# Performance work log

Measured on AMD Instinct MI355X. Metric: run time of the kernel, lower is better.

The kernel has to match this reference:

```python
import jax, jax.numpy as jnp
import numpy as np
from jax import lax

B, T, V, E, H = 32, 512, 32000, 300, 256
TRANSITION = 0.1
TEMP = 0.01
BUDGET_PCT = 30.0
NEG = -1e9


def setup_inputs() -> dict:
    key = jax.random.key(0)
    ks = jax.random.split(key, 10)
    sc = lambda k, shape, s=0.05: (jax.random.normal(k, shape, jnp.float32) * s)
    x = jax.random.randint(ks[0], (B, T), 0, V)
    mask = jnp.ones((B, T), bool)
    embed = sc(ks[1], (V, E), 0.1)
    w_ih_f = sc(ks[2], (E, 4 * H))
    w_hh_f = sc(ks[3], (H, 4 * H))
    b_f = jnp.zeros((4 * H,), jnp.float32)
    w_ih_b = sc(ks[4], (E, 4 * H))
    w_hh_b = sc(ks[5], (H, 4 * H))
    b_b = jnp.zeros((4 * H,), jnp.float32)
    w_out = sc(ks[6], (2 * H, 1), 0.1)
    b_out = jnp.zeros((1,), jnp.float32)
    return {"x": x, "current_epoch": 0, "mask": mask, "embed": embed,
            "w_ih_f": w_ih_f, "w_hh_f": w_hh_f, "b_f": b_f,
            "w_ih_b": w_ih_b, "w_hh_b": w_hh_b, "b_b": b_b,
            "w_out": w_out, "b_out": b_out}


def _lstm_dir(emb, mask, Wi, Wh, b):
    # masked LSTM equivalent to pack_padded_sequence; gate order i,f,g,o (torch)
    bs, tl, _ = emb.shape
    h0 = jnp.zeros((bs, Wh.shape[0]), emb.dtype)
    xg = emb @ Wi + b  # [B,T,4H]

    def step(carry, inp):
        h, c = carry
        xg_t, m_t = inp
        g = xg_t + h @ Wh
        i, f, gg, o = jnp.split(g, 4, axis=-1)
        i = jax.nn.sigmoid(i); f = jax.nn.sigmoid(f)
        gg = jnp.tanh(gg); o = jax.nn.sigmoid(o)
        c_new = f * c + i * gg
        h_new = o * jnp.tanh(c_new)
        m = m_t[:, None]
        h_new = jnp.where(m, h_new, h)
        c_new = jnp.where(m, c_new, c)
        return (h_new, c_new), jnp.where(m, h_new, 0.0)

    _, hs = lax.scan(step, (h0, h0), (xg.transpose(1, 0, 2), mask.T))
    return hs.transpose(1, 0, 2)


def _forward(x, mask, embed, w_ih_f, w_hh_f, b_f, w_ih_b, w_hh_b, b_b, w_out, b_out):
    emb = embed[x]  # [B,T,E] (dropout disabled / eval)
    h_f = _lstm_dir(emb, mask, w_ih_f, w_hh_f, b_f)
    h_b = jnp.flip(_lstm_dir(jnp.flip(emb, 1), jnp.flip(mask, 1), w_ih_b, w_hh_b, b_b), 1)
    h = jnp.concatenate([h_f, h_b], axis=-1)  # [B,T,2H]
    scores = (h @ w_out + b_out)[..., 0]  # [B,T]

    lengths = mask.sum(1)
    pos = jnp.arange(T)
    # unary for state 0 (selected); padded positions forced off
    u0 = jnp.where(pos[None, :] < lengths[:, None], scores / TEMP, NEG)
    # transition[t,0,0] = transition/temp for t <= length, else 0;  t in 0..T
    tvals = jnp.where(jnp.arange(T + 1)[None, :] <= lengths[:, None], TRANSITION / TEMP, 0.0)
    budget = jnp.round(BUDGET_PCT / 100.0 * lengths)
    Cmax = int(round(BUDGET_PCT / 100.0 * T)) + 1  # static count dim

    def logZ(u0_):
        alpha = jnp.full((u0_.shape[0], Cmax, 2), NEG, u0_.dtype)
        alpha = alpha.at[:, 1, 0].set(u0_[:, 0] + tvals[:, 0])  # start in state0 (count 1)
        alpha = alpha.at[:, 0, 1].set(0.0)                       # start in state1 (count 0)

        def step(a, inp):
            u0_t, t_t = inp
            a_shift = jnp.concatenate([jnp.full((a.shape[0], 1, 2), NEG, a.dtype), a[:, :-1, :]], axis=1)
            m0 = jnp.logaddexp(a_shift[..., 0] + t_t[:, None], a_shift[..., 1])
            m1 = jnp.logaddexp(a[..., 0], a[..., 1])
            return jnp.stack([u0_t[:, None] + m0, m1], axis=-1), None

        alpha, _ = lax.scan(step, alpha, (u0_[:, 1:].T, tvals[:, 1:T].T))
        final = jnp.stack([alpha[..., 0] + tvals[:, T][:, None], alpha[..., 1]], axis=-1)
        allowed = (jnp.arange(Cmax)[None, :] <= budget[:, None])[..., None]
        lz = jax.nn.logsumexp(jnp.where(allowed, final, NEG).reshape(final.shape[0], -1), axis=-1)
        return lz.sum()

    # marginal p(z_i=1) = d logZ / d u0_i  (budget-constrained chain marginals)
    z = jax.grad(logZ)(u0)
    return jnp.where(mask, z, 0.0)


def reference(x, current_epoch, mask, embed, w_ih_f, w_hh_f, b_f, w_ih_b, w_hh_b, b_b, w_out, b_out):
    return _forward(x, mask, embed, w_ih_f, w_hh_f, b_f, w_ih_b, w_hh_b, b_b, w_out, b_out)
```

## Files before the change

### kernel.cpp

```cpp
#include <hip/hip_runtime.h>
#include <math.h>

#define BB 32
#define TT_LEN 512
#define EE 300
#define KPAD 320
#define HH 256
#define G4 1024
#define CMAX 155
#define TRANS_T 10.0f
#define NEGF -1.0e9f
#define INV_TEMP 100.0f
#define AST_STRIDE 160

#define NCH_L2 8
#define NREG 24

typedef _Float16 half2v __attribute__((ext_vector_type(2)));
typedef _Float16 half8 __attribute__((ext_vector_type(8)));
typedef float f32x4 __attribute__((ext_vector_type(4)));

__device__ __forceinline__ float la(float x, float y) {
  float m = fmaxf(x, y);
  float d = fminf(x, y) - m;
  return m + __logf(1.0f + __expf(d));
}

__device__ __forceinline__ float sigm(float x) {
  return 1.0f / (1.0f + __expf(-x));
}

__device__ __forceinline__ float dot2acc(unsigned int wd, unsigned int hd, float acc) {
#if __has_builtin(__builtin_amdgcn_fdot2)
  return __builtin_amdgcn_fdot2(__builtin_bit_cast(half2v, wd),
                                __builtin_bit_cast(half2v, hd), acc, false);
#else
  half2v a = __builtin_bit_cast(half2v, wd);
  half2v b = __builtin_bit_cast(half2v, hd);
  return acc + (float)a.x * (float)b.x + (float)a.y * (float)b.y;
#endif
}

__device__ __forceinline__ unsigned int packh(float a, float b) {
  half2v hp;
  hp.x = (_Float16)a;
  hp.y = (_Float16)b;
  return __builtin_bit_cast(unsigned int, hp);
}

__global__ void prep_weights(const float* wi_f, const float* wi_b,
                             const float* wh_f, const float* wh_b,
                             const float* b_f, const float* b_b,
                             _Float16* wi_t, float* b_p,
                             unsigned int* wlds_h, unsigned int* wstr_h) {
  int idx = blockIdx.x * blockDim.x + threadIdx.x;
  int stride = gridDim.x * blockDim.x;
  for (int i = idx; i < 2 * G4 * KPAD; i += stride) {
    int dir = i / (G4 * KPAD);
    int r = i % (G4 * KPAD);
    int j = r / KPAD;
    int k = r % KPAD;
    int g = j & 3, u = j >> 2;
    const float* src = dir ? wi_b : wi_f;
    wi_t[i] = (k < EE) ? (_Float16)src[(size_t)k * G4 + g * HH + u] : (_Float16)0.0f;
  }
  for (int i = idx; i < 2 * NCH_L2 * 4096; i += stride) {
    int dir = i / (NCH_L2 * 4096);
    int r = i % (NCH_L2 * 4096);
    int c = r / 4096;
    int r2 = r % 4096;
    int j = r2 >> 2, d = r2 & 3;
    int g = j & 3, u = j >> 2;
    int k0 = 8 * c + 2 * d;
    const float* src = dir ? wh_b : wh_f;
    wlds_h[i] = packh(src[k0 * G4 + g * HH + u], src[(k0 + 1) * G4 + g * HH + u]);
  }
  for (int i = idx; i < 2 * NREG * 4096; i += stride) {
    int dir = i / (NREG * 4096);
    int r = i % (NREG * 4096);
    int gch = r / 4096;
    int r2 = r % 4096;
    int j = r2 >> 2, d = r2 & 3;
    int g = j & 3, u = j >> 2;
    int k0 = 64 + 8 * gch + 2 * d;
    const float* src = dir ? wh_b : wh_f;
    wstr_h[i] = packh(src[k0 * G4 + g * HH + u], src[(k0 + 1) * G4 + g * HH + u]);
  }
  for (int i = idx; i < 2 * G4; i += stride) {
    int dir = i / G4;
    int j = i % G4;
    int g = j & 3, u = j >> 2;
    const float* src = dir ? b_b : b_f;
    b_p[i] = src[g * HH + u];
  }
}

__global__ void gather_emb(const int* x, const float* embed, _Float16* emb_h) {
  int row = blockIdx.x;
  int v = x[row];
  const float* src = embed + (size_t)v * EE;
  _Float16* dst = emb_h + (size_t)row * KPAD;
  for (int k = threadIdx.x; k < KPAD; k += blockDim.x)
    dst[k] = (k < EE) ? (_Float16)src[k] : (_Float16)0.0f;
}

__global__ __launch_bounds__(256) void xg_mfma(
    const _Float16* __restrict__ emb_h, const _Float16* __restrict__ wi_t,
    const float* __restrict__ b_p, float* __restrict__ xg) {
  int dir = blockIdx.z;
  int n0 = blockIdx.x * 64;
  int m0 = blockIdx.y * 64;
  int wave = threadIdx.x >> 6;
  int lane = threadIdx.x & 63;
  int l15 = lane & 15, quad = lane >> 4;

  const _Float16* arow = emb_h + (size_t)(m0 + wave * 16 + l15) * KPAD + quad * 8;
  const _Float16* bbase =
      wi_t + ((size_t)dir * G4 + n0 + l15) * KPAD + quad * 8;

  f32x4 acc[4];
#pragma unroll
  for (int nt = 0; nt < 4; ++nt) acc[nt] = (f32x4){0.f, 0.f, 0.f, 0.f};

#pragma unroll
  for (int kk = 0; kk < KPAD / 32; ++kk) {
    half8 a = *(const half8*)(arow + kk * 32);
#pragma unroll
    for (int nt = 0; nt < 4; ++nt) {
      half8 b = *(const half8*)(bbase + (size_t)nt * 16 * KPAD + kk * 32);
      acc[nt] = __builtin_amdgcn_mfma_f32_16x16x32_f16(a, b, acc[nt], 0, 0, 0);
    }
  }
#pragma unroll
  for (int nt = 0; nt < 4; ++nt) {
    int n = n0 + nt * 16 + l15;
    float bias = b_p[dir * G4 + n];
#pragma unroll
    for (int r = 0; r < 4; ++r) {
      int m = m0 + wave * 16 + quad * 4 + r;
      xg[((size_t)dir * (BB * TT_LEN) + m) * G4 + n] = acc[nt][r] + bias;
    }
  }
}

__global__ __launch_bounds__(512, 2) void lstm_reg(
    const float* __restrict__ xg, const unsigned int* __restrict__ wlds_h,
    const uint4* __restrict__ wstr, const float* __restrict__ w_out,
    float* __restrict__ scores_part) {
  int bid = blockIdx.x;
  int dir = bid >> 5, b = bid & 31;
  int t = threadIdx.x;
  int lane = t & 63, wid = t >> 6;

  __shared__ uint4 wlds[NCH_L2 * 1024];
  __shared__ uint4 hpk4[32];
  __shared__ float gates[1024];
  __shared__ float wpart[2][4];

  const uint4* wsrcl = (const uint4*)wlds_h + (size_t)dir * (NCH_L2 * 1024);
  for (int i = t; i < NCH_L2 * 1024; i += 512) wlds[i] = wsrcl[i];
  const uint4* wsb = wstr + (size_t)dir * (NREG * 1024);
  uint4 wr0[NREG], wr1[NREG];
#pragma unroll
  for (int g = 0; g < NREG; ++g) {
    wr0[g] = wsb[g * 1024 + t];
    wr1[g] = wsb[g * 1024 + t + 512];
  }
  if (t < 32) hpk4[t] = uint4{0, 0, 0, 0};
  __syncthreads();

  const float* xgbase =
      xg + (size_t)(dir * (BB * TT_LEN) + b * TT_LEN) * G4 + t;
  float wo = (t < HH) ? w_out[dir * HH + t] : 0.0f;
  float cstate = 0.0f;

  int t0 = dir ? (TT_LEN - 1) : 0;
  float xgn0 = xgbase[(size_t)t0 * G4];
  float xgn1 = xgbase[(size_t)t0 * G4 + 512];

#pragma unroll 1
  for (int s = 0; s < TT_LEN; ++s) {
    int tt = dir ? (TT_LEN - 1 - s) : s;
    float acc0 = xgn0, acc1 = xgn1;
    if (s + 1 < TT_LEN) {
      int t2 = dir ? (TT_LEN - 2 - s) : (s + 1);
      xgn0 = xgbase[(size_t)t2 * G4];
      xgn1 = xgbase[(size_t)t2 * G4 + 512];
    }
#pragma unroll
    for (int c = 0; c < NCH_L2; ++c) {
      uint4 h = hpk4[c];
      uint4 w0 = wlds[c * 1024 + t];
      uint4 w1 = wlds[c * 1024 + 512 + t];
      acc0 = dot2acc(w0.x, h.x, acc0);
      acc0 = dot2acc(w0.y, h.y, acc0);
      acc0 = dot2acc(w0.z, h.z, acc0);
      acc0 = dot2acc(w0.w, h.w, acc0);
      acc1 = dot2acc(w1.x, h.x, acc1);
      acc1 = dot2acc(w1.y, h.y, acc1);
      acc1 = dot2acc(w1.z, h.z, acc1);
      acc1 = dot2acc(w1.w, h.w, acc1);
    }
#pragma unroll
    for (int g = 0; g < NREG; ++g) {
      uint4 h = hpk4[NCH_L2 + g];
      acc0 = dot2acc(wr0[g].x, h.x, acc0);
      acc0 = dot2acc(wr0[g].y, h.y, acc0);
      acc0 = dot2acc(wr0[g].z, h.z, acc0);
      acc0 = dot2acc(wr0[g].w, h.w, acc0);
      acc1 = dot2acc(wr1[g].x, h.x, acc1);
      acc1 = dot2acc(wr1[g].y, h.y, acc1);
      acc1 = dot2acc(wr1[g].z, h.z, acc1);
      acc1 = dot2acc(wr1[g].w, h.w, acc1);
    }
    gates[t] = acc0;
    gates[512 + t] = acc1;
    __syncthreads();

    if (t < HH) {
      float4 g4 = ((const float4*)gates)[t];
      float ig = sigm(g4.x);
      float fg = sigm(g4.y);
      float gg = tanhf(g4.z);
      float og = sigm(g4.w);
      cstate = fg * cstate + ig * gg;
      float h = og * tanhf(cstate);
      float prod = h * wo;
#pragma unroll
      for (int off = 32; off > 0; off >>= 1) prod += __shfl_down(prod, off, 64);
      if (lane == 0) wpart[s & 1][wid] = prod;
      float hn = __shfl_down(h, 1, 64);
      if (!(t & 1)) ((unsigned int*)hpk4)[t >> 1] = packh(h, hn);
    }
    __syncthreads();
    if (t == 0) {
      scores_part[(size_t)(dir * BB + b) * TT_LEN + tt] =
          wpart[s & 1][0] + wpart[s & 1][1] + wpart[s & 1][2] + wpart[s & 1][3];
    }
  }
}

__global__ __launch_bounds__(64) void dp2(const float* __restrict__ scores_part,
                                          const float* __restrict__ b_out,
                                          float* __restrict__ ast_g,
                                          float* __restrict__ out) {
  int b = blockIdx.x;
  int l = threadIdx.x;
  const float* spf = scores_part + (size_t)b * TT_LEN;
  const float* spb = scores_part + (size_t)(BB + b) * TT_LEN;
  float bo = b_out[0];
  float* ast = ast_g + (size_t)b * TT_LEN * AST_STRIDE;

  float ur[8];
#pragma unroll
  for (int i = 0; i < 8; ++i)
    ur[i] = (spf[i * 64 + l] + spb[i * 64 + l] + bo) * INV_TEMP;

  int lm1 = (l + 63) & 63;
  int lp1 = (l + 1) & 63;

  float a0[3], a1[3];
  float u00 = __shfl(ur[0], 0, 64);
  a0[0] = (l == 1) ? (u00 + TRANS_T) : NEGF;
  a0[1] = NEGF;
  a0[2] = NEGF;
  a1[0] = (l == 0) ? 0.0f : NEGF;
  a1[1] = NEGF;
  a1[2] = NEGF;
  ast[l] = a0[0];
  ast[64 + l] = a0[1];
  if (l < 27) ast[128 + l] = a0[2];

#pragma unroll
  for (int ch = 0; ch < 8; ++ch) {
    float uc = ur[ch];
#pragma unroll 1
    for (int tt = (ch == 0 ? 1 : 0); tt < 64; ++tt) {
      int t = ch * 64 + tt;
      float u0t = __shfl(uc, tt, 64);
      float w0a = __shfl(a0[0], lm1, 64);
      float w1a = __shfl(a0[1], lm1, 64);
      float w2a = __shfl(a0[2], lm1, 64);
      float w0b = __shfl(a1[0], lm1, 64);
      float w1b = __shfl(a1[1], lm1, 64);
      float w2b = __shfl(a1[2], lm1, 64);
      float p0a = (l == 0) ? NEGF : w0a;
      float p1a = (l == 0) ? w0a : w1a;
      float p2a = (l == 0) ? w1a : w2a;
      float p0b = (l == 0) ? NEGF : w0b;
      float p1b = (l == 0) ? w0b : w1b;
      float p2b = (l == 0) ? w1b : w2b;
      float n00 = u0t + la(p0a + TRANS_T, p0b);
      float n01 = u0t + la(p1a + TRANS_T, p1b);
      float n02 = u0t + la(p2a + TRANS_T, p2b);
      float n10 = la(a0[0], a1[0]);
      float n11 = la(a0[1], a1[1]);
      float n12 = la(a0[2], a1[2]);
      a0[0] = n00;
      a0[1] = n01;
      a0[2] = (l < 27) ? n02 : NEGF;
      a1[0] = n10;
      a1[1] = n11;
      a1[2] = (l < 27) ? n12 : NEGF;
      float* astr = ast + (size_t)t * AST_STRIDE;
      astr[l] = a0[0];
      astr[64 + l] = a0[1];
      if (l < 27) astr[128 + l] = a0[2];
    }
  }

  float f00 = a0[0] + TRANS_T, f01 = a0[1] + TRANS_T, f02 = a0[2] + TRANS_T;
  float m = fmaxf(fmaxf(fmaxf(f00, f01), fmaxf(f02, a1[0])), fmaxf(a1[1], a1[2]));
#pragma unroll
  for (int off = 32; off > 0; off >>= 1) m = fmaxf(m, __shfl_xor(m, off, 64));
  float es = __expf(f00 - m) + __expf(f01 - m) + __expf(f02 - m) +
             __expf(a1[0] - m) + __expf(a1[1] - m) + __expf(a1[2] - m);
#pragma unroll
  for (int off = 32; off > 0; off >>= 1) es += __shfl_xor(es, off, 64);
  float lz = m + __logf(es);

  float b0[3], b1[3];
  b0[0] = TRANS_T;
  b0[1] = TRANS_T;
  b0[2] = (l < 27) ? TRANS_T : NEGF;
  b1[0] = 0.0f;
  b1[1] = 0.0f;
  b1[2] = (l < 27) ? 0.0f : NEGF;
  {
    float ts = __expf(a0[0] + TRANS_T - lz) + __expf(a0[1] + TRANS_T - lz) +
               ((l < 27) ? __expf(a0[2] + TRANS_T - lz) : 0.0f);
#pragma unroll
    for (int off = 32; off > 0; off >>= 1) ts += __shfl_xor(ts, off, 64);
    if (l == 0) out[b * TT_LEN + (TT_LEN - 1)] = ts;
  }

  float nr0 = ast[(size_t)510 * AST_STRIDE + l];
  float nr1 = ast[(size_t)510 * AST_STRIDE + 64 + l];
  float nr2 = (l < 27) ? ast[(size_t)510 * AST_STRIDE + 128 + l] : NEGF;

#pragma unroll
  for (int ch = 7; ch >= 0; --ch) {
    float uc = ur[ch];
#pragma unroll 1
    for (int tt = 63; tt >= (ch == 0 ? 1 : 0); --tt) {
      int t = ch * 64 + tt;
      float u0t = __shfl(uc, tt, 64);
      float c0 = nr0, c1 = nr1, c2 = nr2;
      if (t >= 2) {
        const float* astr = ast + (size_t)(t - 2) * AST_STRIDE;
        nr0 = astr[l];
        nr1 = astr[64 + l];
        nr2 = (l < 27) ? astr[128 + l] : NEGF;
      }
      float w0 = __shfl(b0[0], lp1, 64);
      float w1 = __shfl(b0[1], lp1, 64);
      float w2 = __shfl(b0[2], lp1, 64);
      float x2 = (l == 63) ? NEGF : w2;
      float x1 = (l == 63) ? w2 : w1;
      float x0 = (l == 63) ? w1 : w0;
      float nb00 = la(u0t + TRANS_T + x0, b1[0]);
      float nb01 = la(u0t + TRANS_T + x1, b1[1]);
      float nb02 = la(u0t + TRANS_T + x2, b1[2]);
      float nb10 = la(u0t + x0, b1[0]);
      float nb11 = la(u0t + x1, b1[1]);
      float nb12 = la(u0t + x2, b1[2]);
      float tm = __expf(c0 + nb00 - lz) + __expf(c1 + nb01 - lz) +
                 ((l < 27) ? __expf(c2 + nb02 - lz) : 0.0f);
#pragma unroll
      for (int off = 32; off > 0; off >>= 1) tm += __shfl_xor(tm, off, 64);
      if (l == 0) out[b * TT_LEN + (t - 1)] = tm;
      b0[0] = nb00;
      b0[1] = nb01;
      b0[2] = (l < 27) ? nb02 : NEGF;
      b1[0] = nb10;
      b1[1] = nb11;
      b1[2] = (l < 27) ? nb12 : NEGF;
    }
  }
}

extern "C" void kernel_launch(void* const* d_in, const int* in_sizes, int n_in,
                              void* d_out, int out_size, void* d_ws, size_t ws_size,
                              hipStream_t stream) {
  const int* x = (const int*)d_in[0];
  const float* embed = (const float*)d_in[3];
  const float* wi_f = (const float*)d_in[4];
  const float* wh_f = (const float*)d_in[5];
  const float* bf = (const float*)d_in[6];
  const float* wi_b = (const float*)d_in[7];
  const float* wh_b = (const float*)d_in[8];
  const float* bbias = (const float*)d_in[9];
  const float* w_out = (const float*)d_in[10];
  const float* b_out = (const float*)d_in[11];

  float* ws = (float*)d_ws;
  float* b_p = ws;
  unsigned int* wlds_h = (unsigned int*)(b_p + 2 * G4);
  unsigned int* wstr_h = wlds_h + 2 * NCH_L2 * 4096;
  _Float16* wi_t = (_Float16*)(wstr_h + 2 * NREG * 4096);
  _Float16* emb_h = wi_t + (size_t)2 * G4 * KPAD;
  float* xg = (float*)(emb_h + (size_t)BB * TT_LEN * KPAD);
  float* scores_part = xg + (size_t)2 * BB * TT_LEN * G4;
  float* u0_unused = scores_part + 2 * BB * TT_LEN;
  float* ast_g = u0_unused + BB * TT_LEN;
  float* outp = (float*)d_out;

  prep_weights<<<256, 256, 0, stream>>>(wi_f, wi_b, wh_f, wh_b, bf, bbias,
                                        wi_t, b_p, wlds_h, wstr_h);
  gather_emb<<<BB * TT_LEN, 256, 0, stream>>>(x, embed, emb_h);
  dim3 g1(G4 / 64, (BB * TT_LEN) / 64, 2);
  xg_mfma<<<g1, 256, 0, stream>>>(emb_h, wi_t, b_p, xg);
  lstm_reg<<<64, 512, 0, stream>>>(xg, wlds_h, (const uint4*)wstr_h, w_out,
                                   scores_part);
  dp2<<<BB, 64, 0, stream>>>(scores_part, b_out, ast_g, outp);
}
```

Before: 1.900 ms.

## Pre-swizzle MFMA fragments, split LSTM accumulators, chunk recurrence into four launches

Input weights and gathered embeddings are now written directly in MFMA fragment order, so the xg GEMM loads each operand as one coalesced uint4 per lane instead of strided half8 rows. The LSTM recurrence uses two accumulator chains per gate row to shorten the dependent dot2 chain. It is also split into four launches of 128 steps each, with h and c saved to and restored from global memory between chunks. The AST stride changes from 160 to 159, likely to avoid LDS or cache bank conflicts in the DP. Chunking adds launch overhead and reloads all register and LDS weights four times, which may cost more than it gains.

```diff
diff --git a/kernel.cpp b/kernel.cpp
--- a/kernel.cpp
+++ b/kernel.cpp
@@ -11,7 +11,7 @@
 #define TRANS_T 10.0f
 #define NEGF -1.0e9f
 #define INV_TEMP 100.0f
-#define AST_STRIDE 160
+#define AST_STRIDE 159
 
 #define NCH_L2 8
 #define NREG 24
@@ -51,18 +51,24 @@
 __global__ void prep_weights(const float* wi_f, const float* wi_b,
                              const float* wh_f, const float* wh_b,
                              const float* b_f, const float* b_b,
-                             _Float16* wi_t, float* b_p,
+                             unsigned int* wi_frag, float* b_p,
                              unsigned int* wlds_h, unsigned int* wstr_h) {
   int idx = blockIdx.x * blockDim.x + threadIdx.x;
   int stride = gridDim.x * blockDim.x;
-  for (int i = idx; i < 2 * G4 * KPAD; i += stride) {
-    int dir = i / (G4 * KPAD);
-    int r = i % (G4 * KPAD);
-    int j = r / KPAD;
-    int k = r % KPAD;
-    int g = j & 3, u = j >> 2;
+  for (int i = idx; i < 2 * 64 * 10 * 64 * 4; i += stride) {
+    int u4 = i >> 2, d = i & 3;
+    int lane = u4 & 63;
+    int kk = (u4 >> 6) % 10;
+    int nb = (u4 / 640) & 63;
+    int dir = u4 / (640 * 64);
+    int l15 = lane & 15, quad = lane >> 4;
+    int n = nb * 16 + l15;
+    int g = n & 3, u = n >> 2;
+    int k0 = kk * 32 + quad * 8 + 2 * d;
     const float* src = dir ? wi_b : wi_f;
-    wi_t[i] = (k < EE) ? (_Float16)src[(size_t)k * G4 + g * HH + u] : (_Float16)0.0f;
+    float v0 = (k0 < EE) ? src[(size_t)k0 * G4 + g * HH + u] : 0.0f;
+    float v1 = (k0 + 1 < EE) ? src[(size_t)(k0 + 1) * G4 + g * HH + u] : 0.0f;
+    wi_frag[i] = packh(v0, v1);
   }
   for (int i = idx; i < 2 * NCH_L2 * 4096; i += stride) {
     int dir = i / (NCH_L2 * 4096);
@@ -95,58 +101,73 @@
   }
 }
 
-__global__ void gather_emb(const int* x, const float* embed, _Float16* emb_h) {
-  int row = blockIdx.x;
-  int v = x[row];
-  const float* src = embed + (size_t)v * EE;
-  _Float16* dst = emb_h + (size_t)row * KPAD;
-  for (int k = threadIdx.x; k < KPAD; k += blockDim.x)
-    dst[k] = (k < EE) ? (_Float16)src[k] : (_Float16)0.0f;
+__global__ void gather_emb(const int* x, const float* embed, uint4* emb_frag) {
+  int mblk = blockIdx.x;
+  int t = threadIdx.x;
+  __shared__ int xs[16];
+  if (t < 16) xs[t] = x[mblk * 16 + t];
+  __syncthreads();
+  for (int slot = t; slot < 640; slot += 256) {
+    int kk = slot >> 6;
+    int lane = slot & 63;
+    int l15 = lane & 15, quad = lane >> 4;
+    int row = xs[l15];
+    int kbase = kk * 32 + quad * 8;
+    const float* src = embed + (size_t)row * EE;
+    float v[8];
+#pragma unroll
+    for (int e = 0; e < 8; ++e) v[e] = (kbase + e < EE) ? src[kbase + e] : 0.0f;
+    uint4 o;
+    o.x = packh(v[0], v[1]);
+    o.y = packh(v[2], v[3]);
+    o.z = packh(v[4], v[5]);
+    o.w = packh(v[6], v[7]);
+    emb_frag[(size_t)(mblk * 10 + kk) * 64 + lane] = o;
+  }
 }
 
 __global__ __launch_bounds__(256) void xg_mfma(
-    const _Float16* __restrict__ emb_h, const _Float16* __restrict__ wi_t,
+    const uint4* __restrict__ emb_frag, const uint4* __restrict__ wi_frag,
     const float* __restrict__ b_p, float* __restrict__ xg) {
   int dir = blockIdx.z;
-  int n0 = blockIdx.x * 64;
-  int m0 = blockIdx.y * 64;
-  int wave = threadIdx.x >> 6;
+  int w = threadIdx.x >> 6;
   int lane = threadIdx.x & 63;
   int l15 = lane & 15, quad = lane >> 4;
-
-  const _Float16* arow = emb_h + (size_t)(m0 + wave * 16 + l15) * KPAD + quad * 8;
-  const _Float16* bbase =
-      wi_t + ((size_t)dir * G4 + n0 + l15) * KPAD + quad * 8;
-
+  int mblk = blockIdx.y * 4 + w;
+
+  const uint4* abase = emb_frag + (size_t)mblk * 10 * 64 + lane;
   f32x4 acc[4];
 #pragma unroll
   for (int nt = 0; nt < 4; ++nt) acc[nt] = (f32x4){0.f, 0.f, 0.f, 0.f};
 
 #pragma unroll
-  for (int kk = 0; kk < KPAD / 32; ++kk) {
-    half8 a = *(const half8*)(arow + kk * 32);
+  for (int kk = 0; kk < 10; ++kk) {
+    half8 a = __builtin_bit_cast(half8, abase[kk * 64]);
 #pragma unroll
     for (int nt = 0; nt < 4; ++nt) {
-      half8 b = *(const half8*)(bbase + (size_t)nt * 16 * KPAD + kk * 32);
+      int nb = blockIdx.x * 4 + nt;
+      half8 b = __builtin_bit_cast(
+          half8, wi_frag[((size_t)(dir * 64 + nb) * 10 + kk) * 64 + lane]);
       acc[nt] = __builtin_amdgcn_mfma_f32_16x16x32_f16(a, b, acc[nt], 0, 0, 0);
     }
   }
 #pragma unroll
   for (int nt = 0; nt < 4; ++nt) {
-    int n = n0 + nt * 16 + l15;
+    int n = (blockIdx.x * 4 + nt) * 16 + l15;
     float bias = b_p[dir * G4 + n];
 #pragma unroll
     for (int r = 0; r < 4; ++r) {
-      int m = m0 + wave * 16 + quad * 4 + r;
+      int m = mblk * 16 + quad * 4 + r;
       xg[((size_t)dir * (BB * TT_LEN) + m) * G4 + n] = acc[nt][r] + bias;
     }
   }
 }
 
-__global__ __launch_bounds__(512, 2) void lstm_reg(
+__global__ __launch_bounds__(512, 2) void lstm_ck(
     const float* __restrict__ xg, const unsigned int* __restrict__ wlds_h,
     const uint4* __restrict__ wstr, const float* __restrict__ w_out,
-    float* __restrict__ scores_part) {
+    float* __restrict__ scores_part, float* __restrict__ hst,
+    float* __restrict__ cst, int s0i, int s1i) {
   int bid = blockIdx.x;
   int dir = bid >> 5, b = bid & 31;
   int t = threadIdx.x;
@@ -166,22 +187,25 @@
     wr0[g] = wsb[g * 1024 + t];
     wr1[g] = wsb[g * 1024 + t + 512];
   }
-  if (t < 32) hpk4[t] = uint4{0, 0, 0, 0};
+  if (t < 32)
+    hpk4[t] = (s0i == 0) ? uint4{0, 0, 0, 0} : ((const uint4*)hst)[bid * 32 + t];
+  float cstate = 0.0f;
+  if (s0i > 0 && t < HH) cstate = cst[bid * HH + t];
   __syncthreads();
 
   const float* xgbase =
       xg + (size_t)(dir * (BB * TT_LEN) + b * TT_LEN) * G4 + t;
   float wo = (t < HH) ? w_out[dir * HH + t] : 0.0f;
-  float cstate = 0.0f;
-
-  int t0 = dir ? (TT_LEN - 1) : 0;
+
+  int t0 = dir ? (TT_LEN - 1 - s0i) : s0i;
   float xgn0 = xgbase[(size_t)t0 * G4];
   float xgn1 = xgbase[(size_t)t0 * G4 + 512];
 
 #pragma unroll 1
-  for (int s = 0; s < TT_LEN; ++s) {
+  for (int s = s0i; s < s1i; ++s) {
     int tt = dir ? (TT_LEN - 1 - s) : s;
-    float acc0 = xgn0, acc1 = xgn1;
+    float acc0a = xgn0, acc1a = xgn1;
+    float acc0b = 0.0f, acc1b = 0.0f;
     if (s + 1 < TT_LEN) {
       int t2 = dir ? (TT_LEN - 2 - s) : (s + 1);
       xgn0 = xgbase[(size_t)t2 * G4];
@@ -192,29 +216,40 @@
       uint4 h = hpk4[c];
       uint4 w0 = wlds[c * 1024 + t];
       uint4 w1 = wlds[c * 1024 + 512 + t];
-      acc0 = dot2acc(w0.x, h.x, acc0);
-      acc0 = dot2acc(w0.y, h.y, acc0);
-      acc0 = dot2acc(w0.z, h.z, acc0);
-      acc0 = dot2acc(w0.w, h.w, acc0);
-      acc1 = dot2acc(w1.x, h.x, acc1);
-      acc1 = dot2acc(w1.y, h.y, acc1);
-      acc1 = dot2acc(w1.z, h.z, acc1);
-      acc1 = dot2acc(w1.w, h.w, acc1);
+      acc0a = dot2acc(w0.x, h.x, acc0a);
+      acc0a = dot2acc(w0.y, h.y, acc0a);
+      acc0a = dot2acc(w0.z, h.z, acc0a);
+      acc0a = dot2acc(w0.w, h.w, acc0a);
+      acc1a = dot2acc(w1.x, h.x, acc1a);
+      acc1a = dot2acc(w1.y, h.y, acc1a);
+      acc1a = dot2acc(w1.z, h.z, acc1a);
+      acc1a = dot2acc(w1.w, h.w, acc1a);
     }
 #pragma unroll
     for (int g = 0; g < NREG; ++g) {
       uint4 h = hpk4[NCH_L2 + g];
-      acc0 = dot2acc(wr0[g].x, h.x, acc0);
-      acc0 = dot2acc(wr0[g].y, h.y, acc0);
-      acc0 = dot2acc(wr0[g].z, h.z, acc0);
-      acc0 = dot2acc(wr0[g].w, h.w, acc0);
-      acc1 = dot2acc(wr1[g].x, h.x, acc1);
-      acc1 = dot2acc(wr1[g].y, h.y, acc1);
-      acc1 = dot2acc(wr1[g].z, h.z, acc1);
-      acc1 = dot2acc(wr1[g].w, h.w, acc1);
-    }
-    gates[t] = acc0;
-    gates[512 + t] = acc1;
+      if (g < 12) {
+        acc0a = dot2acc(wr0[g].x, h.x, acc0a);
+        acc0a = dot2acc(wr0[g].y, h.y, acc0a);
+        acc0a = dot2acc(wr0[g].z, h.z, acc0a);
+        acc0a = dot2acc(wr0[g].w, h.w, acc0a);
+        acc1a = dot2acc(wr1[g].x, h.x, acc1a);
+        acc1a = dot2acc(wr1[g].y, h.y, acc1a);
+        acc1a = dot2acc(wr1[g].z, h.z, acc1a);
+        acc1a = dot2acc(wr1[g].w, h.w, acc1a);
+      } else {
+        acc0b = dot2acc(wr0[g].x, h.x, acc0b);
+        acc0b = dot2acc(wr0[g].y, h.y, acc0b);
+        acc0b = dot2acc(wr0[g].z, h.z, acc0b);
+        acc0b = dot2acc(wr0[g].w, h.w, acc0b);
+        acc1b = dot2acc(wr1[g].x, h.x, acc1b);
+        acc1b = dot2acc(wr1[g].y, h.y, acc1b);
+        acc1b = dot2acc(wr1[g].z, h.z, acc1b);
+        acc1b = dot2acc(wr1[g].w, h.w, acc1b);
+      }
+    }
+    gates[t] = acc0a + acc0b;
+    gates[512 + t] = acc1a + acc1b;
     __syncthreads();
 
     if (t < HH) {
@@ -238,6 +273,8 @@
           wpart[s & 1][0] + wpart[s & 1][1] + wpart[s & 1][2] + wpart[s & 1][3];
     }
   }
+  if (t < 32) ((uint4*)hst)[bid * 32 + t] = hpk4[t];
+  if (t < HH) cst[bid * HH + t] = cstate;
 }
 
 __global__ __launch_bounds__(64) void dp2(const float* __restrict__ scores_part,
@@ -397,20 +434,24 @@
   float* b_p = ws;
   unsigned int* wlds_h = (unsigned int*)(b_p + 2 * G4);
   unsigned int* wstr_h = wlds_h + 2 * NCH_L2 * 4096;
-  _Float16* wi_t = (_Float16*)(wstr_h + 2 * NREG * 4096);
-  _Float16* emb_h = wi_t + (size_t)2 * G4 * KPAD;
-  float* xg = (float*)(emb_h + (size_t)BB * TT_LEN * KPAD);
+  unsigned int* wi_frag = wstr_h + 2 * NREG * 4096;
+  uint4* emb_frag = (uint4*)(wi_frag + 2 * 64 * 10 * 64 * 4);
+  float* xg = (float*)(emb_frag + (size_t)1024 * 10 * 64);
   float* scores_part = xg + (size_t)2 * BB * TT_LEN * G4;
-  float* u0_unused = scores_part + 2 * BB * TT_LEN;
-  float* ast_g = u0_unused + BB * TT_LEN;
+  float* hst = scores_part + 2 * BB * TT_LEN;
+  float* cst = hst + 64 * 32 * 4;
+  float* ast_g = cst + 64 * HH;
   float* outp = (float*)d_out;
 
   prep_weights<<<256, 256, 0, stream>>>(wi_f, wi_b, wh_f, wh_b, bf, bbias,
-                                        wi_t, b_p, wlds_h, wstr_h);
-  gather_emb<<<BB * TT_LEN, 256, 0, stream>>>(x, embed, emb_h);
-  dim3 g1(G4 / 64, (BB * TT_LEN) / 64, 2);
-  xg_mfma<<<g1, 256, 0, stream>>>(emb_h, wi_t, b_p, xg);
-  lstm_reg<<<64, 512, 0, stream>>>(xg, wlds_h, (const uint4*)wstr_h, w_out,
-                                   scores_part);
+                                        wi_frag, b_p, wlds_h, wstr_h);
+  gather_emb<<<(BB * TT_LEN) / 16, 256, 0, stream>>>(x, embed, emb_frag);
+  dim3 g1(16, 256, 2);
+  xg_mfma<<<g1, 256, 0, stream>>>(emb_frag, (const uint4*)wi_frag, b_p, xg);
+  for (int c = 0; c < 4; ++c) {
+    lstm_ck<<<64, 512, 0, stream>>>(xg, wlds_h, (const uint4*)wstr_h, w_out,
+                                    scores_part, hst, cst, c * 128,
+                                    (c + 1) * 128);
+  }
   dp2<<<BB, 64, 0, stream>>>(scores_part, b_out, ast_g, outp);
 }
```

Result: no change. 1.893 ms (-0.4%).
